# Performance work log

Measured on AMD Instinct MI355X. Metric: run time of the kernel, lower is better.

Reference implementation:

```python
import jax, jax.numpy as jnp
import numpy as np
from jax import lax

T, B, S = 64, 32, 64
V, E, H = 32000, 512, 512

def _p(key, shape, scale=0.05):
    return (jax.random.normal(key, shape, dtype=jnp.float32) * scale)

def setup_inputs() -> dict:
    key = jax.random.key(0)
    ks = jax.random.split(key, 24)
    inp = {
        'trg': jax.random.randint(ks[0], (T, B), 0, V),
        'encoded_src': jax.random.normal(ks[1], (S, B, 2 * H), dtype=jnp.float32),
        'emb': _p(ks[2], (V, E)),
        # LSTM layer 0: input = E + 2H
        'W_ih0': _p(ks[3], (4 * H, E + 2 * H)), 'W_hh0': _p(ks[4], (4 * H, H)),
        'b_ih0': _p(ks[5], (4 * H,)), 'b_hh0': _p(ks[6], (4 * H,)),
        # LSTM layer 1: input = H
        'W_ih1': _p(ks[7], (4 * H, H)), 'W_hh1': _p(ks[8], (4 * H, H)),
        'b_ih1': _p(ks[9], (4 * H,)), 'b_hh1': _p(ks[10], (4 * H,)),
        # attn_annot: 2H -> H
        'Wa': _p(ks[11], (H, 2 * H)), 'ba': _p(ks[12], (H,)),
        # attn_hidden: H -> H
        'Wh': _p(ks[13], (H, H)), 'bh': _p(ks[14], (H,)),
        # other: H -> 1
        'Wo': _p(ks[15], (1, H)), 'bo': _p(ks[16], (1,)),
        # penult: 3H -> E
        'Wp': _p(ks[17], (E, 3 * H)), 'bp': _p(ks[18], (E,)),
        # out bias (weight tied to emb)
        'b_out': _p(ks[19], (V,)),
    }
    return inp

def _lstm_cell(x, h, c, W_ih, W_hh, b_ih, b_hh):
    # PyTorch gate order: i, f, g, o
    g = x @ W_ih.T + b_ih + h @ W_hh.T + b_hh
    i, f, gg, o = jnp.split(g, 4, axis=-1)
    c_new = jax.nn.sigmoid(f) * c + jax.nn.sigmoid(i) * jnp.tanh(gg)
    h_new = jax.nn.sigmoid(o) * jnp.tanh(c_new)
    return h_new, c_new

def reference(trg, encoded_src, emb, W_ih0, W_hh0, b_ih0, b_hh0,
              W_ih1, W_hh1, b_ih1, b_hh1, Wa, ba, Wh, bh, Wo, bo,
              Wp, bp, b_out):
    trg_emb = emb[trg]                                # [T,B,E]
    annot_scores = encoded_src @ Wa.T + ba            # [S,B,H]
    Hd = W_hh0.shape[1]
    Bd = encoded_src.shape[1]
    h0 = jnp.zeros((2, Bd, Hd), dtype=encoded_src.dtype)
    c0 = jnp.zeros((2, Bd, Hd), dtype=encoded_src.dtype)
    ctx0 = jnp.zeros((Bd, encoded_src.shape[2]), dtype=encoded_src.dtype)

    def step(carry, emb_t):
        h, c, ctx = carry
        x = jnp.concatenate([emb_t, ctx], axis=1)      # [B, E+2H]
        h0n, c0n = _lstm_cell(x,   h[0], c[0], W_ih0, W_hh0, b_ih0, b_hh0)
        h1n, c1n = _lstm_cell(h0n, h[1], c[1], W_ih1, W_hh1, b_ih1, b_hh1)
        out = h1n                                      # [B,H]
        hs = out @ Wh.T + bh                           # [B,H]
        e = jnp.tanh(hs[None] + annot_scores) @ Wo.T + bo   # [S,B,1]
        a = jax.nn.softmax(e, axis=0)[..., 0]          # [S,B]
        ctx_new = jnp.einsum('sb,sbd->bd', a, encoded_src)  # [B,2H]
        stacked = jnp.concatenate([out, ctx_new], axis=1)   # [B,3H]
        return (jnp.stack([h0n, h1n]), jnp.stack([c0n, c1n]), ctx_new), stacked

    (h, c, _), all_scores = lax.scan(step, (h0, c0, ctx0), trg_emb)  # all_scores [T,B,3H]
    pen = all_scores @ Wp.T + bp                       # [T,B,E]
    logits = pen @ emb.T + b_out                       # [T,B,V] (tied weights)
    scores = jax.nn.log_softmax(logits, axis=2)
    return (scores, h, c)
```

## Files before the change

### kernel.cpp

```cpp
#include <hip/hip_runtime.h>


typedef unsigned short u16;
typedef short bf16x8 __attribute__((ext_vector_type(8)));
typedef float f32x4 __attribute__((ext_vector_type(4)));

#define MFMA_BF16(a, b, c) __builtin_amdgcn_mfma_f32_16x16x32_bf16((a), (b), (c), 0, 0, 0)

struct __attribute__((aligned(8))) U16x4 { u16 x, y, z, w; };

__device__ __forceinline__ float b2f(u16 u) {
  unsigned v = ((unsigned)u) << 16; float f; __builtin_memcpy(&f, &v, 4); return f;
}
__device__ __forceinline__ u16 f2b(float f) {
  unsigned u; __builtin_memcpy(&u, &f, 4);
  u = (u + 0x7FFFu + ((u >> 16) & 1u)) >> 16;
  return (u16)u;
}
__device__ __forceinline__ float sigm(float x) { return 1.f / (1.f + __expf(-x)); }
__device__ __forceinline__ float tanh_fast(float x) {
  x = fminf(fmaxf(x, -15.f), 15.f);
  float e = __expf(2.f * x);
  return (e - 1.f) / (e + 1.f);
}

__device__ __forceinline__ bf16x8 bl16(const u16* p) {
  bf16x8 v;
  asm volatile("global_load_dwordx4 %0, %1, off sc0 sc1" : "=v"(v) : "v"(p) : "memory");
  return v;
}
__device__ __forceinline__ float blf(const float* p) {
  float v;
  asm volatile("global_load_dword %0, %1, off sc0 sc1" : "=v"(v) : "v"(p) : "memory");
  return v;
}
__device__ __forceinline__ u16 blu16(const u16* p) {
  unsigned v;
  asm volatile("global_load_ushort %0, %1, off sc0 sc1" : "=v"(v) : "v"(p) : "memory");
  return (u16)v;
}
__device__ __forceinline__ void bs16(u16* p, u16 d) {
  unsigned dd = d;
  asm volatile("global_store_short %0, %1, off sc0 sc1" :: "v"(p), "v"(dd) : "memory");
}
__device__ __forceinline__ void bs32(float* p, float d) {
  asm volatile("global_store_dword %0, %1, off sc0 sc1" :: "v"(p), "v"(d) : "memory");
}
__device__ __forceinline__ void bs32u(u16* p, unsigned d) {
  asm volatile("global_store_dword %0, %1, off sc0 sc1" :: "v"(p), "v"(d) : "memory");
}
__device__ __forceinline__ void vmwait() {
  asm volatile("s_waitcnt vmcnt(0)" ::: "memory");
  __builtin_amdgcn_sched_barrier(0);
}

__global__ void f2b4_kernel(const float* __restrict__ src, u16* __restrict__ dst, long n4) {
  long i = (long)blockIdx.x * blockDim.x + threadIdx.x;
  long stride = (long)gridDim.x * blockDim.x;
  for (; i < n4; i += stride) {
    float4 v = ((const float4*)src)[i];
    U16x4 o; o.x = f2b(v.x); o.y = f2b(v.y); o.z = f2b(v.z); o.w = f2b(v.w);
    ((U16x4*)dst)[i] = o;
  }
}

__global__ void f2b4_strided(const float* __restrict__ src, u16* __restrict__ dst,
                             int rows, int cols4, int sld, int soff, int dld, int doff) {
  int total = rows * cols4;
  for (int i = blockIdx.x * blockDim.x + threadIdx.x; i < total; i += gridDim.x * blockDim.x) {
    int r = i / cols4, c4 = i - r * cols4;
    float4 v = *(const float4*)(src + (size_t)r * sld + soff + c4 * 4);
    U16x4 o; o.x = f2b(v.x); o.y = f2b(v.y); o.z = f2b(v.z); o.w = f2b(v.w);
    *(U16x4*)(dst + (size_t)r * dld + doff + c4 * 4) = o;
  }
}

__global__ void gather_emb_kernel(const int* __restrict__ trg, const float* __restrict__ emb,
                                  u16* __restrict__ out) {
  int r = blockIdx.x;
  int v = trg[r];
  const float* srow = emb + (size_t)v * 512;
  u16* drow = out + (size_t)r * 512;
  for (int e = threadIdx.x; e < 128; e += blockDim.x) {
    float4 x = ((const float4*)srow)[e];
    U16x4 o; o.x = f2b(x.x); o.y = f2b(x.y); o.z = f2b(x.z); o.w = f2b(x.w);
    ((U16x4*)drow)[e] = o;
  }
}

__global__ void annot_tr_kernel(const float* __restrict__ annot, u16* __restrict__ abt) {
  int b = blockIdx.x >> 6, s = blockIdx.x & 63;
  const float* src = annot + (size_t)(s * 32 + b) * 512;
  u16* dst = abt + (size_t)(b * 64 + s) * 512;
  int j = threadIdx.x;
  float4 v = ((const float4*)src)[j];
  U16x4 o; o.x = f2b(v.x); o.y = f2b(v.y); o.z = f2b(v.z); o.w = f2b(v.w);
  ((U16x4*)dst)[j] = o;
}

__global__ void enc_tr_kernel(const float* __restrict__ enc, u16* __restrict__ ebt) {
  int b = blockIdx.x >> 6, s = blockIdx.x & 63;
  const float* src = enc + (size_t)(s * 32 + b) * 1024;
  u16* dst = ebt + (size_t)(b * 64 + s) * 1024;
  int j = threadIdx.x;
  float4 v = ((const float4*)src)[j];
  U16x4 o; o.x = f2b(v.x); o.y = f2b(v.y); o.z = f2b(v.z); o.w = f2b(v.w);
  ((U16x4*)dst)[j] = o;
}

template <int MODE>
__global__ __launch_bounds__(256) void gemm_bt(
    const u16* __restrict__ A, const u16* __restrict__ B,
    float* __restrict__ outF, u16* __restrict__ outB,
    const float* __restrict__ bias0, const float* __restrict__ bias1,
    int N, int K, int ntiles, float* __restrict__ pmax, float* __restrict__ psum) {
  const int l = threadIdx.x & 63, wv = threadIdx.x >> 6;
  const int m0 = blockIdx.x * 128 + wv * 32;
  const int n0 = blockIdx.y * 64;
  const int kg = ((l >> 4) << 3);
  const u16* Ap0 = A + (size_t)(m0 + (l & 15)) * K + kg;
  const u16* Ap1 = Ap0 + (size_t)16 * K;
  const u16* Bp = B + (size_t)(n0 + (l & 15)) * K + kg;
  f32x4 acc[2][4] = {};
  for (int k0 = 0; k0 < K; k0 += 32) {
    bf16x8 a0 = *(const bf16x8*)(Ap0 + k0);
    bf16x8 a1 = *(const bf16x8*)(Ap1 + k0);
#pragma unroll
    for (int nf = 0; nf < 4; ++nf) {
      bf16x8 bb = *(const bf16x8*)(Bp + (size_t)(nf * 16) * K + k0);
      acc[0][nf] = MFMA_BF16(a0, bb, acc[0][nf]);
      acc[1][nf] = MFMA_BF16(a1, bb, acc[1][nf]);
    }
  }
  float biasv[4];
#pragma unroll
  for (int nf = 0; nf < 4; ++nf) {
    int col = n0 + nf * 16 + (l & 15);
    float bv = bias0 ? bias0[col] : 0.f;
    if (bias1) bv += bias1[col];
    biasv[nf] = bv;
  }
#pragma unroll
  for (int mi = 0; mi < 2; ++mi)
#pragma unroll
    for (int nf = 0; nf < 4; ++nf)
#pragma unroll
      for (int i = 0; i < 4; ++i) acc[mi][nf][i] += biasv[nf];

#pragma unroll
  for (int mi = 0; mi < 2; ++mi)
#pragma unroll
    for (int i = 0; i < 4; ++i) {
      int row = m0 + mi * 16 + ((l >> 4) << 2) + i;
#pragma unroll
      for (int nf = 0; nf < 4; ++nf) {
        int col = n0 + nf * 16 + (l & 15);
        if constexpr (MODE == 1)
          outB[(size_t)row * N + col] = f2b(acc[mi][nf][i]);
        else
          outF[(size_t)row * N + col] = acc[mi][nf][i];
      }
    }
  if constexpr (MODE == 2) {
    float lm[2][4], se[2][4];
#pragma unroll
    for (int mi = 0; mi < 2; ++mi)
#pragma unroll
      for (int i = 0; i < 4; ++i) {
        float m_ = acc[mi][0][i];
#pragma unroll
        for (int nf = 1; nf < 4; ++nf) m_ = fmaxf(m_, acc[mi][nf][i]);
        lm[mi][i] = m_;
      }
#pragma unroll
    for (int d = 1; d < 16; d <<= 1)
#pragma unroll
      for (int mi = 0; mi < 2; ++mi)
#pragma unroll
        for (int i = 0; i < 4; ++i) lm[mi][i] = fmaxf(lm[mi][i], __shfl_xor(lm[mi][i], d));
#pragma unroll
    for (int mi = 0; mi < 2; ++mi)
#pragma unroll
      for (int i = 0; i < 4; ++i) {
        float s_ = 0.f;
#pragma unroll
        for (int nf = 0; nf < 4; ++nf) s_ += __expf(acc[mi][nf][i] - lm[mi][i]);
        se[mi][i] = s_;
      }
#pragma unroll
    for (int d = 1; d < 16; d <<= 1)
#pragma unroll
      for (int mi = 0; mi < 2; ++mi)
#pragma unroll
        for (int i = 0; i < 4; ++i) se[mi][i] += __shfl_xor(se[mi][i], d);
    if ((l & 15) == 0) {
#pragma unroll
      for (int mi = 0; mi < 2; ++mi)
#pragma unroll
        for (int i = 0; i < 4; ++i) {
          int row = m0 + mi * 16 + ((l >> 4) << 2) + i;
          pmax[(size_t)row * ntiles + blockIdx.y] = lm[mi][i];
          psum[(size_t)row * ntiles + blockIdx.y] = se[mi][i];
        }
    }
  }
}

__device__ __forceinline__ void grid_barrier(unsigned* flags, unsigned phase) {
  __syncthreads();
  if (threadIdx.x == 0) {
    __hip_atomic_store(flags + blockIdx.x * 32, phase, __ATOMIC_RELAXED,
                       __HIP_MEMORY_SCOPE_AGENT);
  }
  if (threadIdx.x < 32) {
    int spins = 0;
    while (__hip_atomic_load(flags + threadIdx.x * 32, __ATOMIC_RELAXED,
                             __HIP_MEMORY_SCOPE_AGENT) < phase &&
           spins < 2000000) ++spins;
  }
  __syncthreads();
}

__global__ __launch_bounds__(512, 2) void scan_kernel(
    const u16* __restrict__ xW0,
    const u16* __restrict__ Wcat0,
    const u16* __restrict__ Wcat1,
    const u16* __restrict__ Whb,
    const float* __restrict__ b_ih1, const float* __restrict__ b_hh1,
    const float* __restrict__ bh, const float* __restrict__ Wo, const float* __restrict__ bo,
    const u16* __restrict__ annot_bt,
    const u16* __restrict__ enc_bt,
    u16* __restrict__ ctxb,
    u16* __restrict__ h0b,
    u16* __restrict__ h1b,
    float* __restrict__ c0, float* __restrict__ c1,
    float* __restrict__ hs,
    u16* __restrict__ scoresb,
    float* __restrict__ dout_hc,
    unsigned* __restrict__ flags) {
  __shared__ float sm[16384];
  const int w = blockIdx.x;
  const int tid = threadIdx.x;
  const int l = tid & 63, wv = tid >> 6;
  const int jh0 = w * 16;
  const int bE = tid >> 4, jlE = tid & 15;
  unsigned phase = 0;

  float gb1[4];
#pragma unroll
  for (int g = 0; g < 4; ++g) gb1[g] = b_ih1[g * 512 + jh0 + jlE] + b_hh1[g * 512 + jh0 + jlE];
  const float bhv = bh[jh0 + jlE];
  const float bov = bo[0];

  for (int t = 0; t < 64; ++t) {
    const int pA = t & 1;
    {
      const int kg = ((l >> 4) << 3);
      u16 xw[4];
      {
        const u16* xp = xW0 + (size_t)(t * 32 + bE) * 2048 + jh0 + jlE;
#pragma unroll
        for (int g = 0; g < 4; ++g) xw[g] = blu16(xp + g * 512);
      }
      bf16x8 a0[6], a1[6];
#pragma unroll
      for (int kk = 0; kk < 6; ++kk) {
        const int k0 = wv * 192 + kk * 32;
        const u16* ab; int ld, off;
        if (k0 < 1024) { ab = ctxb; ld = 1024; off = k0; }
        else { ab = h0b + pA * 32 * 512; ld = 512; off = k0 - 1024; }
        a0[kk] = bl16(ab + (size_t)(l & 15) * ld + off + kg);
        a1[kk] = bl16(ab + (size_t)((l & 15) + 16) * ld + off + kg);
      }
      vmwait();
      f32x4 acc[2][4] = {};
#pragma unroll
      for (int kk = 0; kk < 6; ++kk) {
        const int k0 = wv * 192 + kk * 32;
#pragma unroll
        for (int g = 0; g < 4; ++g) {
          bf16x8 bb = *(const bf16x8*)(Wcat0 + (size_t)(g * 512 + jh0 + (l & 15)) * 1536 + k0 + kg);
          acc[0][g] = MFMA_BF16(a0[kk], bb, acc[0][g]);
          acc[1][g] = MFMA_BF16(a1[kk], bb, acc[1][g]);
        }
      }
#pragma unroll
      for (int mi = 0; mi < 2; ++mi)
#pragma unroll
        for (int g = 0; g < 4; ++g)
#pragma unroll
          for (int i = 0; i < 4; ++i) {
            int m = mi * 16 + ((l >> 4) << 2) + i;
            sm[(wv * 32 + m) * 64 + g * 16 + (l & 15)] = acc[mi][g][i];
          }
      __syncthreads();
      {
        const int b = bE, jl = jlE, jh = jh0 + jl;
        float gate[4];
#pragma unroll
        for (int g = 0; g < 4; ++g) {
          float s = 0.f;
#pragma unroll
          for (int kv = 0; kv < 8; ++kv) s += sm[(kv * 32 + b) * 64 + g * 16 + jl];
          gate[g] = s + b2f(xw[g]);
        }
        float cn = sigm(gate[1]) * c0[b * 512 + jh] + sigm(gate[0]) * tanh_fast(gate[2]);
        float hn = sigm(gate[3]) * tanh_fast(cn);
        c0[b * 512 + jh] = cn;
        bs16(h0b + (pA ^ 1) * 32 * 512 + b * 512 + jh, f2b(hn));
        if (t == 63) { dout_hc[b * 512 + jh] = hn; dout_hc[32768 + b * 512 + jh] = cn; }
      }
    }
    grid_barrier(flags, ++phase);
    {
      const int kg = ((l >> 4) << 3);
      bf16x8 a0[4], a1[4];
#pragma unroll
      for (int kk = 0; kk < 4; ++kk) {
        const int k0 = wv * 128 + kk * 32;
        const u16* ab; int off;
        if (k0 < 512) { ab = h0b + (pA ^ 1) * 32 * 512; off = k0; }
        else { ab = h1b + pA * 32 * 512; off = k0 - 512; }
        a0[kk] = bl16(ab + (size_t)(l & 15) * 512 + off + kg);
        a1[kk] = bl16(ab + (size_t)((l & 15) + 16) * 512 + off + kg);
      }
      vmwait();
      f32x4 acc[2][4] = {};
#pragma unroll
      for (int kk = 0; kk < 4; ++kk) {
        const int k0 = wv * 128 + kk * 32;
#pragma unroll
        for (int g = 0; g < 4; ++g) {
          bf16x8 bb = *(const bf16x8*)(Wcat1 + (size_t)(g * 512 + jh0 + (l & 15)) * 1024 + k0 + kg);
          acc[0][g] = MFMA_BF16(a0[kk], bb, acc[0][g]);
          acc[1][g] = MFMA_BF16(a1[kk], bb, acc[1][g]);
        }
      }
#pragma unroll
      for (int mi = 0; mi < 2; ++mi)
#pragma unroll
        for (int g = 0; g < 4; ++g)
#pragma unroll
          for (int i = 0; i < 4; ++i) {
            int m = mi * 16 + ((l >> 4) << 2) + i;
            sm[(wv * 32 + m) * 64 + g * 16 + (l & 15)] = acc[mi][g][i];
          }
      __syncthreads();
      {
        const int b = bE, jl = jlE, jh = jh0 + jl;
        float gate[4];
#pragma unroll
        for (int g = 0; g < 4; ++g) {
          float s = 0.f;
#pragma unroll
          for (int kv = 0; kv < 8; ++kv) s += sm[(kv * 32 + b) * 64 + g * 16 + jl];
          gate[g] = s + gb1[g];
        }
        float cn = sigm(gate[1]) * c1[b * 512 + jh] + sigm(gate[0]) * tanh_fast(gate[2]);
        float hn = sigm(gate[3]) * tanh_fast(cn);
        c1[b * 512 + jh] = cn;
        u16 hb = f2b(hn);
        bs16(h1b + (pA ^ 1) * 32 * 512 + b * 512 + jh, hb);
        bs16(scoresb + (size_t)(t * 32 + b) * 1536 + jh, hb);
        if (t == 63) { dout_hc[16384 + b * 512 + jh] = hn; dout_hc[32768 + 16384 + b * 512 + jh] = cn; }
      }
    }
    grid_barrier(flags, ++phase);
    {
      const int kg = ((l >> 4) << 3);
      const u16* h1n = h1b + (pA ^ 1) * 32 * 512;
      bf16x8 a0[2], a1[2];
#pragma unroll
      for (int kk = 0; kk < 2; ++kk) {
        const int k0 = wv * 64 + kk * 32;
        a0[kk] = bl16(h1n + (size_t)(l & 15) * 512 + k0 + kg);
        a1[kk] = bl16(h1n + (size_t)((l & 15) + 16) * 512 + k0 + kg);
      }
      vmwait();
      f32x4 acc2[2] = {};
#pragma unroll
      for (int kk = 0; kk < 2; ++kk) {
        const int k0 = wv * 64 + kk * 32;
        bf16x8 bb = *(const bf16x8*)(Whb + (size_t)(jh0 + (l & 15)) * 512 + k0 + kg);
        acc2[0] = MFMA_BF16(a0[kk], bb, acc2[0]);
        acc2[1] = MFMA_BF16(a1[kk], bb, acc2[1]);
      }
#pragma unroll
      for (int mi = 0; mi < 2; ++mi)
#pragma unroll
        for (int i = 0; i < 4; ++i)
          sm[(wv * 32 + mi * 16 + ((l >> 4) << 2) + i) * 16 + (l & 15)] = acc2[mi][i];
      __syncthreads();
      {
        const int b = bE, jl = jlE;
        float s = 0.f;
#pragma unroll
        for (int kv = 0; kv < 8; ++kv) s += sm[(kv * 32 + b) * 16 + jl];
        bs32(hs + b * 512 + jh0 + jl, s + bhv);
      }
    }
    grid_barrier(flags, ++phase);
    {
      const int b = w;
      float* hs_s = sm;
      float* wo_s = sm + 512;
      float* red = sm + 1024;
      float* a_s = sm + 1536;
      float hv = blf(hs + b * 512 + tid);
      float wov = Wo[tid];
      vmwait();
      hs_s[tid] = hv;
      wo_s[tid] = wov;
      __syncthreads();
      const int s_ = tid >> 3, ks = tid & 7;
      const u16* arow = annot_bt + (size_t)(b * 64 + s_) * 512 + ks * 64;
      float accv = 0.f;
#pragma unroll
      for (int kk8 = 0; kk8 < 8; ++kk8) {
        bf16x8 av = *(const bf16x8*)(arow + kk8 * 8);
#pragma unroll
        for (int j = 0; j < 8; ++j) {
          int k = ks * 64 + kk8 * 8 + j;
          accv += tanh_fast(hs_s[k] + b2f((u16)av[j])) * wo_s[k];
        }
      }
      red[tid] = accv;
      __syncthreads();
      if (tid < 64) {
        float e = bov;
#pragma unroll
        for (int j = 0; j < 8; ++j) e += red[tid * 8 + j];
        float mx = e;
#pragma unroll
        for (int d = 1; d < 64; d <<= 1) mx = fmaxf(mx, __shfl_xor(mx, d));
        float p = __expf(e - mx);
        float ss = p;
#pragma unroll
        for (int d = 1; d < 64; d <<= 1) ss += __shfl_xor(ss, d);
        a_s[tid] = p / ss;
      }
      __syncthreads();
      float cx0 = 0.f, cx1 = 0.f;
      const u16* erow = enc_bt + (size_t)b * 65536 + tid * 2;
#pragma unroll 8
      for (int s2 = 0; s2 < 64; ++s2) {
        unsigned ev = *(const unsigned*)(erow + (size_t)s2 * 1024);
        float av = a_s[s2];
        cx0 += av * b2f((u16)(ev & 0xFFFFu));
        cx1 += av * b2f((u16)(ev >> 16));
      }
      u16 u0 = f2b(cx0), u1 = f2b(cx1);
      unsigned pk = (unsigned)u0 | ((unsigned)u1 << 16);
      bs32u(ctxb + b * 1024 + tid * 2, pk);
      bs32u(scoresb + (size_t)(t * 32 + b) * 1536 + 512 + tid * 2, pk);
    }
    grid_barrier(flags, ++phase);
  }
}

__global__ __launch_bounds__(256) void lse_kernel(const float* __restrict__ pmax,
                                                  const float* __restrict__ psum,
                                                  float* __restrict__ lse, int nt) {
  __shared__ float red[256];
  const int r = blockIdx.x;
  float m = -3.4e38f;
  for (int j = threadIdx.x; j < nt; j += 256) m = fmaxf(m, pmax[(size_t)r * nt + j]);
  red[threadIdx.x] = m; __syncthreads();
  for (int s = 128; s > 0; s >>= 1) {
    if (threadIdx.x < s) red[threadIdx.x] = fmaxf(red[threadIdx.x], red[threadIdx.x + s]);
    __syncthreads();
  }
  const float M = red[0]; __syncthreads();
  float s_ = 0.f;
  for (int j = threadIdx.x; j < nt; j += 256)
    s_ += psum[(size_t)r * nt + j] * __expf(pmax[(size_t)r * nt + j] - M);
  red[threadIdx.x] = s_; __syncthreads();
  for (int s = 128; s > 0; s >>= 1) {
    if (threadIdx.x < s) red[threadIdx.x] += red[threadIdx.x + s];
    __syncthreads();
  }
  if (threadIdx.x == 0) lse[r] = M + logf(red[0]);
}

__global__ void finalize_kernel(float* __restrict__ out, const float* __restrict__ lse) {
  const long n4 = 16384000;
  for (long i = (long)blockIdx.x * blockDim.x + threadIdx.x; i < n4;
       i += (long)gridDim.x * blockDim.x) {
    float4 v = ((float4*)out)[i];
    float L = lse[i / 8000];
    v.x -= L; v.y -= L; v.z -= L; v.w -= L;
    ((float4*)out)[i] = v;
  }
}

extern "C" void kernel_launch(void* const* d_in, const int* in_sizes, int n_in,
                              void* d_out, int out_size, void* d_ws, size_t ws_size,
                              hipStream_t stream) {
  const int* trg = (const int*)d_in[0];
  const float* enc = (const float*)d_in[1];
  const float* emb = (const float*)d_in[2];
  const float* W_ih0 = (const float*)d_in[3];
  const float* W_hh0 = (const float*)d_in[4];
  const float* b_ih0 = (const float*)d_in[5];
  const float* b_hh0 = (const float*)d_in[6];
  const float* W_ih1 = (const float*)d_in[7];
  const float* W_hh1 = (const float*)d_in[8];
  const float* b_ih1 = (const float*)d_in[9];
  const float* b_hh1 = (const float*)d_in[10];
  const float* Wa = (const float*)d_in[11];
  const float* ba = (const float*)d_in[12];
  const float* Wh = (const float*)d_in[13];
  const float* bh = (const float*)d_in[14];
  const float* Wo = (const float*)d_in[15];
  const float* bo = (const float*)d_in[16];
  const float* Wp = (const float*)d_in[17];
  const float* bp = (const float*)d_in[18];
  const float* b_out = (const float*)d_in[19];
  float* out = (float*)d_out;

  unsigned char* ws = (unsigned char*)d_ws;
  size_t off = 0;
  auto alloc = [&](size_t bytes) -> void* {
    void* p = ws + off; off += (bytes + 255) & ~(size_t)255; return p;
  };
  u16* emb_b = (u16*)alloc(32768000);
  u16* trgemb_b = (u16*)alloc(2097152);
  u16* enc_b = (u16*)alloc(4194304);
  u16* Wemb0_b = (u16*)alloc(2097152);
  u16* Wcat0_b = (u16*)alloc(6291456);
  u16* Wcat1_b = (u16*)alloc(4194304);
  u16* Wa_b = (u16*)alloc(1048576);
  u16* Wh_b = (u16*)alloc(524288);
  u16* Wp_b = (u16*)alloc(1572864);
  u16* xW0_b = (u16*)alloc(8388608);
  float* annot = (float*)alloc(4194304);
  u16* scoresb = (u16*)alloc(6291456);
  u16* pen_b = (u16*)alloc(2097152);
  u16* ctxb = (u16*)alloc(65536);
  u16* h0b = (u16*)alloc(65536);
  u16* h1b = (u16*)alloc(65536);
  float* c0 = (float*)alloc(65536);
  float* c1 = (float*)alloc(65536);
  float* hsbuf = (float*)alloc(65536);
  float* pmax = (float*)alloc(4194304);
  float* psum = (float*)alloc(4194304);
  float* lse = (float*)alloc(8192);
  unsigned* flags = (unsigned*)alloc(4096);
  if (off > ws_size) return;

  u16* annot_bt = (u16*)pmax;
  u16* enc_bt = (u16*)psum;

  hipMemsetAsync(ctxb, 0, 65536, stream);
  hipMemsetAsync(h0b, 0, 65536, stream);
  hipMemsetAsync(h1b, 0, 65536, stream);
  hipMemsetAsync(c0, 0, 65536, stream);
  hipMemsetAsync(c1, 0, 65536, stream);
  hipMemsetAsync(flags, 0, 4096, stream);

  f2b4_kernel<<<1024, 256, 0, stream>>>(emb, emb_b, 4096000);
  f2b4_kernel<<<256, 256, 0, stream>>>(enc, enc_b, 524288);
  f2b4_kernel<<<128, 256, 0, stream>>>(Wa, Wa_b, 131072);
  f2b4_kernel<<<64, 256, 0, stream>>>(Wh, Wh_b, 65536);
  f2b4_kernel<<<128, 256, 0, stream>>>(Wp, Wp_b, 196608);
  f2b4_strided<<<512, 256, 0, stream>>>(W_ih0, Wemb0_b, 2048, 128, 1536, 0, 512, 0);
  f2b4_strided<<<512, 256, 0, stream>>>(W_ih0, Wcat0_b, 2048, 256, 1536, 512, 1536, 0);
  f2b4_strided<<<512, 256, 0, stream>>>(W_hh0, Wcat0_b, 2048, 128, 512, 0, 1536, 1024);
  f2b4_strided<<<512, 256, 0, stream>>>(W_ih1, Wcat1_b, 2048, 128, 512, 0, 1024, 0);
  f2b4_strided<<<512, 256, 0, stream>>>(W_hh1, Wcat1_b, 2048, 128, 512, 0, 1024, 512);
  gather_emb_kernel<<<2048, 128, 0, stream>>>(trg, emb, trgemb_b);
  enc_tr_kernel<<<2048, 256, 0, stream>>>(enc, enc_bt);

  gemm_bt<1><<<dim3(16, 32), 256, 0, stream>>>(trgemb_b, Wemb0_b, nullptr, xW0_b,
                                               b_ih0, b_hh0, 2048, 512, 0, nullptr, nullptr);
  gemm_bt<0><<<dim3(16, 8), 256, 0, stream>>>(enc_b, Wa_b, annot, nullptr,
                                              ba, nullptr, 512, 1024, 0, nullptr, nullptr);
  annot_tr_kernel<<<2048, 128, 0, stream>>>(annot, annot_bt);

  scan_kernel<<<32, 512, 0, stream>>>(xW0_b, Wcat0_b, Wcat1_b, Wh_b, b_ih1, b_hh1, bh, Wo, bo,
                                      annot_bt, enc_bt, ctxb, h0b, h1b, c0, c1, hsbuf, scoresb,
                                      out + 65536000, flags);
  gemm_bt<1><<<dim3(16, 8), 256, 0, stream>>>(scoresb, Wp_b, nullptr, pen_b,
                                              bp, nullptr, 512, 1536, 0, nullptr, nullptr);
  gemm_bt<2><<<dim3(16, 500), 256, 0, stream>>>(pen_b, emb_b, out, nullptr,
                                                b_out, nullptr, 32000, 512, 500, pmax, psum);
  lse_kernel<<<2048, 256, 0, stream>>>(pmax, psum, lse, 500);
  finalize_kernel<<<2048, 256, 0, stream>>>(out, lse);
}
```

Baseline: 2.522 ms.

## Add wider-tile logits kernel with LDS-staged stores and prefetch weights across barriers

Replaces the MODE 2 GEMM with a dedicated logits kernel that uses 128x128 tiles, a swizzled block order for L2 reuse, and LDS staging so the output goes out as coalesced float4 stores. The number of partial max/sum tiles drops from 500 to 250. Inside the scan kernel, the layer-1 LSTM and attention-hidden weight fragments are now loaded while blocks wait at the grid barrier, hiding load latency behind synchronisation. The cost is higher register and LDS use, which may reduce occupancy.

```diff
diff --git a/kernel.cpp b/kernel.cpp
--- a/kernel.cpp
+++ b/kernel.cpp
@@ -43,11 +43,16 @@
   unsigned dd = d;
   asm volatile("global_store_short %0, %1, off sc0 sc1" :: "v"(p), "v"(dd) : "memory");
 }
-__device__ __forceinline__ void bs32(float* p, float d) {
-  asm volatile("global_store_dword %0, %1, off sc0 sc1" :: "v"(p), "v"(d) : "memory");
-}
 __device__ __forceinline__ void bs32u(u16* p, unsigned d) {
   asm volatile("global_store_dword %0, %1, off sc0 sc1" :: "v"(p), "v"(d) : "memory");
+}
+__device__ __forceinline__ void bsf32(float* p, float d) {
+  asm volatile("global_store_dword %0, %1, off sc0 sc1" :: "v"(p), "v"(d) : "memory");
+}
+__device__ __forceinline__ bf16x8 cl16(const u16* p) {
+  bf16x8 v;
+  asm volatile("global_load_dwordx4 %0, %1, off" : "=v"(v) : "v"(p));
+  return v;
 }
 __device__ __forceinline__ void vmwait() {
   asm volatile("s_waitcnt vmcnt(0)" ::: "memory");
@@ -113,7 +118,7 @@
     const u16* __restrict__ A, const u16* __restrict__ B,
     float* __restrict__ outF, u16* __restrict__ outB,
     const float* __restrict__ bias0, const float* __restrict__ bias1,
-    int N, int K, int ntiles, float* __restrict__ pmax, float* __restrict__ psum) {
+    int N, int K) {
   const int l = threadIdx.x & 63, wv = threadIdx.x >> 6;
   const int m0 = blockIdx.x * 128 + wv * 32;
   const int n0 = blockIdx.y * 64;
@@ -143,66 +148,107 @@
 #pragma unroll
   for (int mi = 0; mi < 2; ++mi)
 #pragma unroll
-    for (int nf = 0; nf < 4; ++nf)
-#pragma unroll
-      for (int i = 0; i < 4; ++i) acc[mi][nf][i] += biasv[nf];
-
-#pragma unroll
-  for (int mi = 0; mi < 2; ++mi)
-#pragma unroll
     for (int i = 0; i < 4; ++i) {
       int row = m0 + mi * 16 + ((l >> 4) << 2) + i;
 #pragma unroll
       for (int nf = 0; nf < 4; ++nf) {
         int col = n0 + nf * 16 + (l & 15);
+        float v = acc[mi][nf][i] + biasv[nf];
         if constexpr (MODE == 1)
-          outB[(size_t)row * N + col] = f2b(acc[mi][nf][i]);
+          outB[(size_t)row * N + col] = f2b(v);
         else
-          outF[(size_t)row * N + col] = acc[mi][nf][i];
-      }
-    }
-  if constexpr (MODE == 2) {
-    float lm[2][4], se[2][4];
+          outF[(size_t)row * N + col] = v;
+      }
+    }
+}
+
+__global__ __launch_bounds__(256) void logits_kernel(
+    const u16* __restrict__ A,
+    const u16* __restrict__ B,
+    const float* __restrict__ bias,
+    float* __restrict__ out,
+    float* __restrict__ pmax, float* __restrict__ psum) {
+  __shared__ float smf[128 * 132];
+  const int id = blockIdx.x;
+  const int lin = (id & 7) * 500 + (id >> 3);
+  const int mt = lin & 15, nt = lin >> 4;
+  const int gm = mt * 128, n0 = nt * 128;
+  const int l = threadIdx.x & 63, wv = threadIdx.x >> 6;
+  const int kg = ((l >> 4) << 3);
+  const int m0 = gm + wv * 32;
+
+  const u16* Ap0 = A + (size_t)(m0 + (l & 15)) * 512 + kg;
+  const u16* Ap1 = Ap0 + (size_t)16 * 512;
+  const u16* Bp = B + (size_t)(n0 + (l & 15)) * 512 + kg;
+  f32x4 acc[2][8] = {};
+  for (int k0 = 0; k0 < 512; k0 += 32) {
+    bf16x8 a0 = *(const bf16x8*)(Ap0 + k0);
+    bf16x8 a1 = *(const bf16x8*)(Ap1 + k0);
+#pragma unroll
+    for (int nf = 0; nf < 8; ++nf) {
+      bf16x8 bb = *(const bf16x8*)(Bp + (size_t)(nf * 16) * 512 + k0);
+      acc[0][nf] = MFMA_BF16(a0, bb, acc[0][nf]);
+      acc[1][nf] = MFMA_BF16(a1, bb, acc[1][nf]);
+    }
+  }
+  float bv[8];
+#pragma unroll
+  for (int nf = 0; nf < 8; ++nf) bv[nf] = bias[n0 + nf * 16 + (l & 15)];
+
+  float lm[2][4], se[2][4];
+#pragma unroll
+  for (int mi = 0; mi < 2; ++mi)
+#pragma unroll
+    for (int i = 0; i < 4; ++i) {
+      int rl = wv * 32 + mi * 16 + ((l >> 4) << 2) + i;
+      float m_ = -3.4e38f;
+#pragma unroll
+      for (int nf = 0; nf < 8; ++nf) {
+        float v = acc[mi][nf][i] + bv[nf];
+        acc[mi][nf][i] = v;
+        smf[rl * 132 + nf * 16 + (l & 15)] = v;
+        m_ = fmaxf(m_, v);
+      }
+      lm[mi][i] = m_;
+    }
+#pragma unroll
+  for (int d = 1; d < 16; d <<= 1)
 #pragma unroll
     for (int mi = 0; mi < 2; ++mi)
 #pragma unroll
+      for (int i = 0; i < 4; ++i) lm[mi][i] = fmaxf(lm[mi][i], __shfl_xor(lm[mi][i], d));
+#pragma unroll
+  for (int mi = 0; mi < 2; ++mi)
+#pragma unroll
+    for (int i = 0; i < 4; ++i) {
+      float s_ = 0.f;
+#pragma unroll
+      for (int nf = 0; nf < 8; ++nf) s_ += __expf(acc[mi][nf][i] - lm[mi][i]);
+      se[mi][i] = s_;
+    }
+#pragma unroll
+  for (int d = 1; d < 16; d <<= 1)
+#pragma unroll
+    for (int mi = 0; mi < 2; ++mi)
+#pragma unroll
+      for (int i = 0; i < 4; ++i) se[mi][i] += __shfl_xor(se[mi][i], d);
+  if ((l & 15) == 0) {
+#pragma unroll
+    for (int mi = 0; mi < 2; ++mi)
+#pragma unroll
       for (int i = 0; i < 4; ++i) {
-        float m_ = acc[mi][0][i];
-#pragma unroll
-        for (int nf = 1; nf < 4; ++nf) m_ = fmaxf(m_, acc[mi][nf][i]);
-        lm[mi][i] = m_;
-      }
-#pragma unroll
-    for (int d = 1; d < 16; d <<= 1)
-#pragma unroll
-      for (int mi = 0; mi < 2; ++mi)
-#pragma unroll
-        for (int i = 0; i < 4; ++i) lm[mi][i] = fmaxf(lm[mi][i], __shfl_xor(lm[mi][i], d));
-#pragma unroll
-    for (int mi = 0; mi < 2; ++mi)
-#pragma unroll
-      for (int i = 0; i < 4; ++i) {
-        float s_ = 0.f;
-#pragma unroll
-        for (int nf = 0; nf < 4; ++nf) s_ += __expf(acc[mi][nf][i] - lm[mi][i]);
-        se[mi][i] = s_;
-      }
-#pragma unroll
-    for (int d = 1; d < 16; d <<= 1)
-#pragma unroll
-      for (int mi = 0; mi < 2; ++mi)
-#pragma unroll
-        for (int i = 0; i < 4; ++i) se[mi][i] += __shfl_xor(se[mi][i], d);
-    if ((l & 15) == 0) {
-#pragma unroll
-      for (int mi = 0; mi < 2; ++mi)
-#pragma unroll
-        for (int i = 0; i < 4; ++i) {
-          int row = m0 + mi * 16 + ((l >> 4) << 2) + i;
-          pmax[(size_t)row * ntiles + blockIdx.y] = lm[mi][i];
-          psum[(size_t)row * ntiles + blockIdx.y] = se[mi][i];
-        }
-    }
+        int row = m0 + mi * 16 + ((l >> 4) << 2) + i;
+        pmax[(size_t)row * 250 + nt] = lm[mi][i];
+        psum[(size_t)row * 250 + nt] = se[mi][i];
+      }
+  }
+  __syncthreads();
+#pragma unroll
+  for (int r = 0; r < 128; r += 8) {
+    int row = r + (threadIdx.x >> 5);
+    int c4 = threadIdx.x & 31;
+    float4 v = *(float4*)&smf[row * 132 + c4 * 4];
+    *(float4*)&out[(size_t)(gm + row) * 32000 + n0 + c4 * 4] = v;
   }
 }
 
@@ -268,7 +314,7 @@
         const int k0 = wv * 192 + kk * 32;
         const u16* ab; int ld, off;
         if (k0 < 1024) { ab = ctxb; ld = 1024; off = k0; }
-        else { ab = h0b + pA * 32 * 512; ld = 512; off = k0 - 1024; }
+        else { ab = h0b + pA * 16384; ld = 512; off = k0 - 1024; }
         a0[kk] = bl16(ab + (size_t)(l & 15) * ld + off + kg);
         a1[kk] = bl16(ab + (size_t)((l & 15) + 16) * ld + off + kg);
       }
@@ -307,11 +353,32 @@
         float cn = sigm(gate[1]) * c0[b * 512 + jh] + sigm(gate[0]) * tanh_fast(gate[2]);
         float hn = sigm(gate[3]) * tanh_fast(cn);
         c0[b * 512 + jh] = cn;
-        bs16(h0b + (pA ^ 1) * 32 * 512 + b * 512 + jh, f2b(hn));
+        bs16(h0b + (pA ^ 1) * 16384 + b * 512 + jh, f2b(hn));
         if (t == 63) { dout_hc[b * 512 + jh] = hn; dout_hc[32768 + b * 512 + jh] = cn; }
       }
     }
-    grid_barrier(flags, ++phase);
+    bf16x8 wB[16];
+    {
+      ++phase;
+      __syncthreads();
+      if (tid == 0)
+        __hip_atomic_store(flags + blockIdx.x * 32, phase, __ATOMIC_RELAXED,
+                           __HIP_MEMORY_SCOPE_AGENT);
+      const int kg = ((l >> 4) << 3);
+#pragma unroll
+      for (int kk = 0; kk < 4; ++kk)
+#pragma unroll
+        for (int g = 0; g < 4; ++g)
+          wB[kk * 4 + g] = cl16(Wcat1 + (size_t)(g * 512 + jh0 + (l & 15)) * 1024 +
+                                wv * 128 + kk * 32 + kg);
+      if (tid < 32) {
+        int spins = 0;
+        while (__hip_atomic_load(flags + tid * 32, __ATOMIC_RELAXED,
+                                 __HIP_MEMORY_SCOPE_AGENT) < phase &&
+               spins < 2000000) ++spins;
+      }
+      __syncthreads();
+    }
     {
       const int kg = ((l >> 4) << 3);
       bf16x8 a0[4], a1[4];
@@ -319,8 +386,8 @@
       for (int kk = 0; kk < 4; ++kk) {
         const int k0 = wv * 128 + kk * 32;
         const u16* ab; int off;
-        if (k0 < 512) { ab = h0b + (pA ^ 1) * 32 * 512; off = k0; }
-        else { ab = h1b + pA * 32 * 512; off = k0 - 512; }
+        if (k0 < 512) { ab = h0b + (pA ^ 1) * 16384; off = k0; }
+        else { ab = h1b + pA * 16384; off = k0 - 512; }
         a0[kk] = bl16(ab + (size_t)(l & 15) * 512 + off + kg);
         a1[kk] = bl16(ab + (size_t)((l & 15) + 16) * 512 + off + kg);
       }
@@ -328,12 +395,10 @@
       f32x4 acc[2][4] = {};
 #pragma unroll
       for (int kk = 0; kk < 4; ++kk) {
-        const int k0 = wv * 128 + kk * 32;
 #pragma unroll
         for (int g = 0; g < 4; ++g) {
-          bf16x8 bb = *(const bf16x8*)(Wcat1 + (size_t)(g * 512 + jh0 + (l & 15)) * 1024 + k0 + kg);
-          acc[0][g] = MFMA_BF16(a0[kk], bb, acc[0][g]);
-          acc[1][g] = MFMA_BF16(a1[kk], bb, acc[1][g]);
+          acc[0][g] = MFMA_BF16(a0[kk], wB[kk * 4 + g], acc[0][g]);
+          acc[1][g] = MFMA_BF16(a1[kk], wB[kk * 4 + g], acc[1][g]);
         }
       }
 #pragma unroll
@@ -360,15 +425,33 @@
         float hn = sigm(gate[3]) * tanh_fast(cn);
         c1[b * 512 + jh] = cn;
         u16 hb = f2b(hn);
-        bs16(h1b + (pA ^ 1) * 32 * 512 + b * 512 + jh, hb);
+        bs16(h1b + (pA ^ 1) * 16384 + b * 512 + jh, hb);
         bs16(scoresb + (size_t)(t * 32 + b) * 1536 + jh, hb);
-        if (t == 63) { dout_hc[16384 + b * 512 + jh] = hn; dout_hc[32768 + 16384 + b * 512 + jh] = cn; }
-      }
-    }
-    grid_barrier(flags, ++phase);
+        if (t == 63) { dout_hc[16384 + b * 512 + jh] = hn; dout_hc[49152 + b * 512 + jh] = cn; }
+      }
+    }
+    bf16x8 wC[2];
+    {
+      ++phase;
+      __syncthreads();
+      if (tid == 0)
+        __hip_atomic_store(flags + blockIdx.x * 32, phase, __ATOMIC_RELAXED,
+                           __HIP_MEMORY_SCOPE_AGENT);
+      const int kg = ((l >> 4) << 3);
+#pragma unroll
+      for (int kk = 0; kk < 2; ++kk)
+        wC[kk] = cl16(Whb + (size_t)(jh0 + (l & 15)) * 512 + wv * 64 + kk * 32 + kg);
+      if (tid < 32) {
+        int spins = 0;
+        while (__hip_atomic_load(flags + tid * 32, __ATOMIC_RELAXED,
+                                 __HIP_MEMORY_SCOPE_AGENT) < phase &&
+               spins < 2000000) ++spins;
+      }
+      __syncthreads();
+    }
     {
       const int kg = ((l >> 4) << 3);
-      const u16* h1n = h1b + (pA ^ 1) * 32 * 512;
+      const u16* h1n = h1b + (pA ^ 1) * 16384;
       bf16x8 a0[2], a1[2];
 #pragma unroll
       for (int kk = 0; kk < 2; ++kk) {
@@ -380,10 +463,8 @@
       f32x4 acc2[2] = {};
 #pragma unroll
       for (int kk = 0; kk < 2; ++kk) {
-        const int k0 = wv * 64 + kk * 32;
-        bf16x8 bb = *(const bf16x8*)(Whb + (size_t)(jh0 + (l & 15)) * 512 + k0 + kg);
-        acc2[0] = MFMA_BF16(a0[kk], bb, acc2[0]);
-        acc2[1] = MFMA_BF16(a1[kk], bb, acc2[1]);
+        acc2[0] = MFMA_BF16(a0[kk], wC[kk], acc2[0]);
+        acc2[1] = MFMA_BF16(a1[kk], wC[kk], acc2[1]);
       }
 #pragma unroll
       for (int mi = 0; mi < 2; ++mi)
@@ -396,7 +477,7 @@
         float s = 0.f;
 #pragma unroll
         for (int kv = 0; kv < 8; ++kv) s += sm[(kv * 32 + b) * 16 + jl];
-        bs32(hs + b * 512 + jh0 + jl, s + bhv);
+        bsf32(hs + b * 512 + jh0 + jl, s + bhv);
       }
     }
     grid_barrier(flags, ++phase);
@@ -449,8 +530,7 @@
         cx0 += av * b2f((u16)(ev & 0xFFFFu));
         cx1 += av * b2f((u16)(ev >> 16));
       }
-      u16 u0 = f2b(cx0), u1 = f2b(cx1);
-      unsigned pk = (unsigned)u0 | ((unsigned)u1 << 16);
+      unsigned pk = (unsigned)f2b(cx0) | ((unsigned)f2b(cx1) << 16);
       bs32u(ctxb + b * 1024 + tid * 2, pk);
       bs32u(scoresb + (size_t)(t * 32 + b) * 1536 + 512 + tid * 2, pk);
     }
@@ -572,18 +652,17 @@
   enc_tr_kernel<<<2048, 256, 0, stream>>>(enc, enc_bt);
 
   gemm_bt<1><<<dim3(16, 32), 256, 0, stream>>>(trgemb_b, Wemb0_b, nullptr, xW0_b,
-                                               b_ih0, b_hh0, 2048, 512, 0, nullptr, nullptr);
+                                               b_ih0, b_hh0, 2048, 512);
   gemm_bt<0><<<dim3(16, 8), 256, 0, stream>>>(enc_b, Wa_b, annot, nullptr,
-                                              ba, nullptr, 512, 1024, 0, nullptr, nullptr);
+                                              ba, nullptr, 512, 1024);
   annot_tr_kernel<<<2048, 128, 0, stream>>>(annot, annot_bt);
 
   scan_kernel<<<32, 512, 0, stream>>>(xW0_b, Wcat0_b, Wcat1_b, Wh_b, b_ih1, b_hh1, bh, Wo, bo,
                                       annot_bt, enc_bt, ctxb, h0b, h1b, c0, c1, hsbuf, scoresb,
                                       out + 65536000, flags);
   gemm_bt<1><<<dim3(16, 8), 256, 0, stream>>>(scoresb, Wp_b, nullptr, pen_b,
-                                              bp, nullptr, 512, 1536, 0, nullptr, nullptr);
-  gemm_bt<2><<<dim3(16, 500), 256, 0, stream>>>(pen_b, emb_b, out, nullptr,
-                                                b_out, nullptr, 32000, 512, 500, pmax, psum);
-  lse_kernel<<<2048, 256, 0, stream>>>(pmax, psum, lse, 500);
+                                              bp, nullptr, 512, 1536);
+  logits_kernel<<<4000, 256, 0, stream>>>(pen_b, emb_b, b_out, out, pmax, psum);
+  lse_kernel<<<2048, 256, 0, stream>>>(pmax, psum, lse, 250);
   finalize_kernel<<<2048, 256, 0, stream>>>(out, lse);
 }
```

Measured after the change: 2.418 ms. 4.2% less time.
